# Kernel optimization log

Hardware: AMD Instinct MI355X
Metric: run time of the kernel (lower is better)

## Reference

```python
import jax, jax.numpy as jnp
import numpy as np

B, N, F_IN, F_OUT = 16, 1024, 128, 128
LEAKY_SLOPE = 0.01  # torch nn.LeakyReLU default


def setup_inputs() -> dict:
    key = jax.random.key(0)
    k1, k2, k3, k4 = jax.random.split(key, 4)
    node_mat = jax.random.normal(k1, (B, N, F_IN), dtype=jnp.float32)
    adj_mat = jax.random.uniform(k2, (B, N, N), dtype=jnp.float32)
    # nn.Linear(node_in_len, node_out_len): weight [F_OUT, F_IN], bias [F_OUT]
    bound = 1.0 / np.sqrt(F_IN)
    W = jax.random.uniform(k3, (F_OUT, F_IN), minval=-bound, maxval=bound, dtype=jnp.float32)
    b = jax.random.uniform(k4, (F_OUT,), minval=-bound, maxval=bound, dtype=jnp.float32)
    return {"node_mat": node_mat, "adj_mat": adj_mat, "W": W, "b": b}


def reference(node_mat, adj_mat, W, b):
    # degree normalization: row-scale adjacency by 1/degree
    # (the torch code builds a diagonal inv-degree matrix and bmm's it;
    #  mathematically identical to a broadcast row scale)
    n_neighbors = adj_mat.sum(axis=-1, keepdims=True)          # [B, N, 1]
    norm_adj = adj_mat / n_neighbors                           # [B, N, N]
    node_fea = jnp.einsum('bnm,bmf->bnf', norm_adj, node_mat)  # [B, N, F_in]
    node_fea = jnp.einsum('bnf,of->bno', node_fea, W) + b      # linear
    return jnp.where(node_fea >= 0, node_fea, LEAKY_SLOPE * node_fea)
```

## Files before the change

### kernel.cpp

```cpp
#include <hip/hip_runtime.h>
#include <hip/hip_bf16.h>


typedef __attribute__((ext_vector_type(8))) __bf16 bf16x8;
typedef __attribute__((ext_vector_type(4))) float f32x4;

__device__ __forceinline__ unsigned f2bf_pk(float lo, float hi) {
    union { float f; unsigned u; } a, b;
    a.f = lo; b.f = hi;
    unsigned ra = (a.u + 0x7FFFu + ((a.u >> 16) & 1u)) >> 16;
    unsigned rb = (b.u + 0x7FFFu + ((b.u >> 16) & 1u)) & 0xFFFF0000u;
    return ra | rb;
}

__device__ __forceinline__ bf16x8 cvt8(const f32x4& a, const f32x4& b) {
    union { unsigned u[4]; bf16x8 v; } r;
    r.u[0] = f2bf_pk(a.x, a.y);
    r.u[1] = f2bf_pk(a.z, a.w);
    r.u[2] = f2bf_pk(b.x, b.y);
    r.u[3] = f2bf_pk(b.z, b.w);
    return r.v;
}

__global__ __launch_bounds__(256, 2)
void k1_xw(const float* __restrict__ x, const float* __restrict__ W,
           unsigned short* __restrict__ yF)
{
    __shared__ unsigned short Ax[32 * 128];
    __shared__ unsigned short Bw[128 * 128];

    const int t  = threadIdx.x;
    const int wg = blockIdx.x;
    const int b  = wg >> 5;
    const int m0 = (wg & 31) << 5;
    const float* xb = x + (((long)b << 10) + m0) * 128;

#pragma unroll
    for (int i = 0; i < 4; ++i) {
        int e = i * 1024 + t * 4;
        int r = e >> 7, f = e & 127;
        f32x4 v = *(const f32x4*)(xb + (long)r * 128 + f);
        int c = f >> 3;
        int byte = r * 256 + (((c ^ (r & 7)) << 4) | ((f & 7) << 1));
        uint2 pk; pk.x = f2bf_pk(v.x, v.y); pk.y = f2bf_pk(v.z, v.w);
        *(uint2*)((char*)Ax + byte) = pk;
    }
#pragma unroll
    for (int i = 0; i < 16; ++i) {
        int e = i * 1024 + t * 4;
        int r = e >> 7, f = e & 127;
        f32x4 v = *(const f32x4*)(W + r * 128 + f);
        int c = f >> 3;
        int byte = r * 256 + (((c ^ (r & 7)) << 4) | ((f & 7) << 1));
        uint2 pk; pk.x = f2bf_pk(v.x, v.y); pk.y = f2bf_pk(v.z, v.w);
        *(uint2*)((char*)Bw + byte) = pk;
    }
    __syncthreads();

    const int lane = t & 63, w = t >> 6;
    const int wm = w >> 1, wn = w & 1;
    const int lrow = lane & 15, lq = lane >> 4;

    bf16x8 af[4];
#pragma unroll
    for (int kk = 0; kk < 4; ++kk) {
        int r = wm * 16 + lrow;
        int c = kk * 4 + lq;
        af[kk] = *(const bf16x8*)((const char*)Ax + r * 256 + ((c ^ (r & 7)) << 4));
    }

    f32x4 zero = {0.f, 0.f, 0.f, 0.f};
    f32x4 acc[4] = {zero, zero, zero, zero};
#pragma unroll
    for (int nf = 0; nf < 4; ++nf) {
#pragma unroll
        for (int kk = 0; kk < 4; ++kk) {
            int o = wn * 64 + nf * 16 + lrow;
            int c = kk * 4 + lq;
            bf16x8 bfrag = *(const bf16x8*)((const char*)Bw + o * 256 + ((c ^ (o & 7)) << 4));
            acc[nf] = __builtin_amdgcn_mfma_f32_16x16x32_bf16(af[kk], bfrag, acc[nf], 0, 0, 0);
        }
    }

    {
        const int ks = m0 >> 5;
        const int q  = wm * 2 + (lq >> 1);
        const int jb = (lq & 1) * 4;
#pragma unroll
        for (int nf = 0; nf < 4; ++nf) {
            int ot = wn * 4 + nf;
            uint2 pk;
            pk.x = f2bf_pk(acc[nf][0], acc[nf][1]);
            pk.y = f2bf_pk(acc[nf][2], acc[nf][3]);
            long off = (((long)(b * 32 + ks) * 8 + ot) << 10) + (q * 16 + lrow) * 8 + jb;
            *(uint2*)(yF + off) = pk;
        }
    }
}

__global__ __launch_bounds__(256, 4)
void k2_agg(const float* __restrict__ adj, const unsigned short* __restrict__ yF,
            const float* __restrict__ bias, float* __restrict__ out)
{
    __shared__ float accbuf[4][16 * 132];
    __shared__ float degw[4][16];

    const int bid = blockIdx.x;
    const int xcd = bid & 7;
    const int j   = bid >> 3;
    const int b   = xcd * 2 + (j >> 6);
    const int n0  = (j & 63) << 4;

    const int t = threadIdx.x;
    const int lane = t & 63, w = t >> 6;
    const int lrow = lane & 15, lq = lane >> 4;

    const float* adjr = adj + ((long)(b * 1024 + n0 + lrow)) * 1024 + lq * 8;
    const unsigned short* fr = yF + (((long)(b * 32 + w * 8) * 8) << 10) + lane * 8;

    f32x4 zero = {0.f, 0.f, 0.f, 0.f};
    f32x4 acc[8] = {zero, zero, zero, zero, zero, zero, zero, zero};
    float dsum = 0.f;

    const int kbase = w << 8;
    f32x4 v0 = *(const f32x4*)(adjr + kbase);
    f32x4 v1 = *(const f32x4*)(adjr + kbase + 4);
#pragma unroll
    for (int kk = 0; kk < 8; ++kk) {
        bf16x8 bb[8];
#pragma unroll
        for (int ot = 0; ot < 8; ++ot)
            bb[ot] = *(const bf16x8*)(fr + ((kk * 8 + ot) << 10));

        f32x4 n0v = zero, n1v = zero;
        if (kk < 7) {
            n0v = *(const f32x4*)(adjr + kbase + (kk + 1) * 32);
            n1v = *(const f32x4*)(adjr + kbase + (kk + 1) * 32 + 4);
        }

        dsum += v0.x + v0.y + v0.z + v0.w + v1.x + v1.y + v1.z + v1.w;
        bf16x8 a = cvt8(v0, v1);
#pragma unroll
        for (int ot = 0; ot < 8; ++ot)
            acc[ot] = __builtin_amdgcn_mfma_f32_16x16x32_bf16(a, bb[ot], acc[ot], 0, 0, 0);

        v0 = n0v; v1 = n1v;
    }

    dsum += __shfl_xor(dsum, 16, 64);
    dsum += __shfl_xor(dsum, 32, 64);
    if (lq == 0) degw[w][lrow] = dsum;

#pragma unroll
    for (int ot = 0; ot < 8; ++ot)
#pragma unroll
        for (int i = 0; i < 4; ++i)
            accbuf[w][(lq * 4 + i) * 132 + ot * 16 + lrow] = acc[ot][i];
    __syncthreads();

    {
        const int n = t >> 4, o0 = (t & 15) * 8;
        float deg = degw[0][n] + degw[1][n] + degw[2][n] + degw[3][n];
        float inv = 1.0f / deg;
        f32x4 s0 = zero, s1 = zero;
#pragma unroll
        for (int ww = 0; ww < 4; ++ww) {
            s0 += *(const f32x4*)&accbuf[ww][n * 132 + o0];
            s1 += *(const f32x4*)&accbuf[ww][n * 132 + o0 + 4];
        }
        f32x4 b0 = *(const f32x4*)(bias + o0);
        f32x4 b1 = *(const f32x4*)(bias + o0 + 4);
        f32x4 r0, r1;
#pragma unroll
        for (int i = 0; i < 4; ++i) {
            float v = s0[i] * inv + b0[i];
            r0[i] = (v >= 0.f) ? v : 0.01f * v;
            float u = s1[i] * inv + b1[i];
            r1[i] = (u >= 0.f) ? u : 0.01f * u;
        }
        float* op = out + (((long)(b * 1024 + n0 + n)) << 7) + o0;
        *(f32x4*)op = r0;
        *(f32x4*)(op + 4) = r1;
    }
}

extern "C" void kernel_launch(void* const* d_in, const int* in_sizes, int n_in,
                              void* d_out, int out_size, void* d_ws, size_t ws_size,
                              hipStream_t stream) {
    const float* node = (const float*)d_in[0];
    const float* adj  = (const float*)d_in[1];
    const float* W    = (const float*)d_in[2];
    const float* bias = (const float*)d_in[3];
    float* out = (float*)d_out;
    unsigned short* yF = (unsigned short*)d_ws;

    k1_xw<<<dim3(512), dim3(256), 0, stream>>>(node, W, yF);
    k2_agg<<<dim3(1024), dim3(256), 0, stream>>>(adj, yF, bias, out);
}
```

Baseline: 31.78 us.

## Enlarge aggregation tile to 64 rows per block to reuse feature fragments

The aggregation kernel now handles 64 adjacency rows per block (four 16-row groups per wave) instead of 16, so each loaded bf16 feature fragment feeds four times as many MFMAs. This cuts redundant reads of the projected features from global memory and halves the blocks in the XW kernel through a matching 64-row tile with an XCD-aware block mapping. In exchange, the grid shrinks to 256 blocks (about one per CU), register pressure rises with 32 accumulators per thread, the explicit adjacency prefetch is dropped, and the epilogue uses scalar LDS reads and 32-wide per-thread stores.

```diff
diff --git a/kernel.cpp b/kernel.cpp
--- a/kernel.cpp
+++ b/kernel.cpp
@@ -26,17 +26,19 @@
 void k1_xw(const float* __restrict__ x, const float* __restrict__ W,
            unsigned short* __restrict__ yF)
 {
-    __shared__ unsigned short Ax[32 * 128];
+    __shared__ unsigned short Ax[64 * 128];
     __shared__ unsigned short Bw[128 * 128];
 
-    const int t  = threadIdx.x;
-    const int wg = blockIdx.x;
-    const int b  = wg >> 5;
-    const int m0 = (wg & 31) << 5;
+    const int t   = threadIdx.x;
+    const int bid = blockIdx.x;
+    const int xcd = bid & 7;
+    const int j   = bid >> 3;
+    const int b   = xcd * 2 + (j >> 4);
+    const int m0  = (j & 15) << 6;
     const float* xb = x + (((long)b << 10) + m0) * 128;
 
 #pragma unroll
-    for (int i = 0; i < 4; ++i) {
+    for (int i = 0; i < 8; ++i) {
         int e = i * 1024 + t * 4;
         int r = e >> 7, f = e & 127;
         f32x4 v = *(const f32x4*)(xb + (long)r * 128 + f);
@@ -58,24 +60,23 @@
     __syncthreads();
 
     const int lane = t & 63, w = t >> 6;
-    const int wm = w >> 1, wn = w & 1;
     const int lrow = lane & 15, lq = lane >> 4;
 
     bf16x8 af[4];
 #pragma unroll
     for (int kk = 0; kk < 4; ++kk) {
-        int r = wm * 16 + lrow;
+        int r = w * 16 + lrow;
         int c = kk * 4 + lq;
         af[kk] = *(const bf16x8*)((const char*)Ax + r * 256 + ((c ^ (r & 7)) << 4));
     }
 
     f32x4 zero = {0.f, 0.f, 0.f, 0.f};
-    f32x4 acc[4] = {zero, zero, zero, zero};
-#pragma unroll
-    for (int nf = 0; nf < 4; ++nf) {
+    f32x4 acc[8] = {zero, zero, zero, zero, zero, zero, zero, zero};
+#pragma unroll
+    for (int nf = 0; nf < 8; ++nf) {
 #pragma unroll
         for (int kk = 0; kk < 4; ++kk) {
-            int o = wn * 64 + nf * 16 + lrow;
+            int o = nf * 16 + lrow;
             int c = kk * 4 + lq;
             bf16x8 bfrag = *(const bf16x8*)((const char*)Bw + o * 256 + ((c ^ (o & 7)) << 4));
             acc[nf] = __builtin_amdgcn_mfma_f32_16x16x32_bf16(af[kk], bfrag, acc[nf], 0, 0, 0);
@@ -83,104 +84,109 @@
     }
 
     {
-        const int ks = m0 >> 5;
-        const int q  = wm * 2 + (lq >> 1);
+        const int ks = (m0 >> 5) + (w >> 1);
+        const int q  = (w & 1) * 2 + (lq >> 1);
         const int jb = (lq & 1) * 4;
 #pragma unroll
-        for (int nf = 0; nf < 4; ++nf) {
-            int ot = wn * 4 + nf;
+        for (int nf = 0; nf < 8; ++nf) {
             uint2 pk;
             pk.x = f2bf_pk(acc[nf][0], acc[nf][1]);
             pk.y = f2bf_pk(acc[nf][2], acc[nf][3]);
-            long off = (((long)(b * 32 + ks) * 8 + ot) << 10) + (q * 16 + lrow) * 8 + jb;
+            long off = (((long)((b * 32 + ks) * 8 + nf)) << 9) + (q * 16 + lrow) * 8 + jb;
             *(uint2*)(yF + off) = pk;
         }
     }
 }
 
-__global__ __launch_bounds__(256, 4)
+__global__ __launch_bounds__(256, 1)
 void k2_agg(const float* __restrict__ adj, const unsigned short* __restrict__ yF,
             const float* __restrict__ bias, float* __restrict__ out)
 {
-    __shared__ float accbuf[4][16 * 132];
-    __shared__ float degw[4][16];
+    __shared__ float accbuf[4][128 * 68];
+    __shared__ float degw[4][64];
 
     const int bid = blockIdx.x;
     const int xcd = bid & 7;
     const int j   = bid >> 3;
-    const int b   = xcd * 2 + (j >> 6);
-    const int n0  = (j & 63) << 4;
+    const int b   = xcd * 2 + (j >> 4);
+    const int n0  = (j & 15) << 6;
 
     const int t = threadIdx.x;
     const int lane = t & 63, w = t >> 6;
     const int lrow = lane & 15, lq = lane >> 4;
 
-    const float* adjr = adj + ((long)(b * 1024 + n0 + lrow)) * 1024 + lq * 8;
-    const unsigned short* fr = yF + (((long)(b * 32 + w * 8) * 8) << 10) + lane * 8;
+    const float* adjr = adj + ((long)(b * 1024 + n0 + lrow)) * 1024 + (w << 8) + lq * 8;
+    const unsigned short* fr = yF + (((long)(b * 32 + w * 8) * 8) << 9) + lane * 8;
 
     f32x4 zero = {0.f, 0.f, 0.f, 0.f};
-    f32x4 acc[8] = {zero, zero, zero, zero, zero, zero, zero, zero};
-    float dsum = 0.f;
-
-    const int kbase = w << 8;
-    f32x4 v0 = *(const f32x4*)(adjr + kbase);
-    f32x4 v1 = *(const f32x4*)(adjr + kbase + 4);
-#pragma unroll
+    f32x4 acc[4][8];
+#pragma unroll
+    for (int rg = 0; rg < 4; ++rg)
+#pragma unroll
+        for (int ot = 0; ot < 8; ++ot) acc[rg][ot] = zero;
+    float ds[4] = {0.f, 0.f, 0.f, 0.f};
+
+#pragma unroll 2
     for (int kk = 0; kk < 8; ++kk) {
+        f32x4 v0[4], v1[4];
+#pragma unroll
+        for (int rg = 0; rg < 4; ++rg) {
+            v0[rg] = *(const f32x4*)(adjr + rg * 16384 + kk * 32);
+            v1[rg] = *(const f32x4*)(adjr + rg * 16384 + kk * 32 + 4);
+        }
         bf16x8 bb[8];
 #pragma unroll
         for (int ot = 0; ot < 8; ++ot)
-            bb[ot] = *(const bf16x8*)(fr + ((kk * 8 + ot) << 10));
-
-        f32x4 n0v = zero, n1v = zero;
-        if (kk < 7) {
-            n0v = *(const f32x4*)(adjr + kbase + (kk + 1) * 32);
-            n1v = *(const f32x4*)(adjr + kbase + (kk + 1) * 32 + 4);
-        }
-
-        dsum += v0.x + v0.y + v0.z + v0.w + v1.x + v1.y + v1.z + v1.w;
-        bf16x8 a = cvt8(v0, v1);
+            bb[ot] = *(const bf16x8*)(fr + ((kk * 8 + ot) << 9));
+
+        bf16x8 a[4];
+#pragma unroll
+        for (int rg = 0; rg < 4; ++rg) {
+            ds[rg] += v0[rg].x + v0[rg].y + v0[rg].z + v0[rg].w
+                    + v1[rg].x + v1[rg].y + v1[rg].z + v1[rg].w;
+            a[rg] = cvt8(v0[rg], v1[rg]);
+        }
+#pragma unroll
+        for (int rg = 0; rg < 4; ++rg)
+#pragma unroll
+            for (int ot = 0; ot < 8; ++ot)
+                acc[rg][ot] = __builtin_amdgcn_mfma_f32_16x16x32_bf16(a[rg], bb[ot], acc[rg][ot], 0, 0, 0);
+    }
+
+#pragma unroll
+    for (int rg = 0; rg < 4; ++rg) {
+        float d = ds[rg];
+        d += __shfl_xor(d, 16, 64);
+        d += __shfl_xor(d, 32, 64);
+        if (lq == 0) degw[w][rg * 16 + lrow] = d;
+    }
+
+#pragma unroll
+    for (int rg = 0; rg < 4; ++rg)
 #pragma unroll
         for (int ot = 0; ot < 8; ++ot)
-            acc[ot] = __builtin_amdgcn_mfma_f32_16x16x32_bf16(a, bb[ot], acc[ot], 0, 0, 0);
-
-        v0 = n0v; v1 = n1v;
-    }
-
-    dsum += __shfl_xor(dsum, 16, 64);
-    dsum += __shfl_xor(dsum, 32, 64);
-    if (lq == 0) degw[w][lrow] = dsum;
-
-#pragma unroll
-    for (int ot = 0; ot < 8; ++ot)
-#pragma unroll
-        for (int i = 0; i < 4; ++i)
-            accbuf[w][(lq * 4 + i) * 132 + ot * 16 + lrow] = acc[ot][i];
+            *(f32x4*)&accbuf[w][(ot * 16 + lrow) * 68 + rg * 16 + lq * 4] = acc[rg][ot];
     __syncthreads();
 
     {
-        const int n = t >> 4, o0 = (t & 15) * 8;
+        const int n = lane;
+        const int o0 = w * 32;
         float deg = degw[0][n] + degw[1][n] + degw[2][n] + degw[3][n];
         float inv = 1.0f / deg;
-        f32x4 s0 = zero, s1 = zero;
-#pragma unroll
-        for (int ww = 0; ww < 4; ++ww) {
-            s0 += *(const f32x4*)&accbuf[ww][n * 132 + o0];
-            s1 += *(const f32x4*)&accbuf[ww][n * 132 + o0 + 4];
-        }
-        f32x4 b0 = *(const f32x4*)(bias + o0);
-        f32x4 b1 = *(const f32x4*)(bias + o0 + 4);
-        f32x4 r0, r1;
-#pragma unroll
-        for (int i = 0; i < 4; ++i) {
-            float v = s0[i] * inv + b0[i];
-            r0[i] = (v >= 0.f) ? v : 0.01f * v;
-            float u = s1[i] * inv + b1[i];
-            r1[i] = (u >= 0.f) ? u : 0.01f * u;
+        float res[32];
+#pragma unroll
+        for (int c = 0; c < 32; ++c) {
+            float s = accbuf[0][(o0 + c) * 68 + n] + accbuf[1][(o0 + c) * 68 + n]
+                    + accbuf[2][(o0 + c) * 68 + n] + accbuf[3][(o0 + c) * 68 + n];
+            float v = s * inv + bias[o0 + c];
+            res[c] = (v >= 0.f) ? v : 0.01f * v;
         }
         float* op = out + (((long)(b * 1024 + n0 + n)) << 7) + o0;
-        *(f32x4*)op = r0;
-        *(f32x4*)(op + 4) = r1;
+#pragma unroll
+        for (int g = 0; g < 8; ++g) {
+            f32x4 r = {res[g * 4], res[g * 4 + 1], res[g * 4 + 2], res[g * 4 + 3]};
+            *(f32x4*)(op + g * 4) = r;
+        }
     }
 }
 
@@ -194,6 +200,6 @@
     float* out = (float*)d_out;
     unsigned short* yF = (unsigned short*)d_ws;
 
-    k1_xw<<<dim3(512), dim3(256), 0, stream>>>(node, W, yF);
-    k2_agg<<<dim3(1024), dim3(256), 0, stream>>>(adj, yF, bias, out);
-}
+    k1_xw<<<dim3(256), dim3(256), 0, stream>>>(node, W, yF);
+    k2_agg<<<dim3(256), dim3(256), 0, stream>>>(adj, yF, bias, out);
+}
```

After: 27.87 us. -12.3%, faster.
